# Kernel tuning notes

Hardware: AMD Instinct MI355X
Metric: run time of the kernel (lower is better)

## Reference

```python
import jax, jax.numpy as jnp
import numpy as np

B, S, H, W = 64, 32, 40, 64
SENS, UNITS, MOTOR, NA = 1283, 48, 4, 2
UNFOLDS = 6  # ncps LTC default ode_unfolds
EPS = 1e-8


def setup_inputs() -> dict:
    key = jax.random.key(0)
    ks = iter(jax.random.split(key, 40))
    u = lambda sh, lo, hi: jax.random.uniform(next(ks), sh, jnp.float32, lo, hi)
    inp = {}
    inp["depth_image"] = jax.random.uniform(next(ks), (B, S, H, W), jnp.float32)
    inp["relative_position"] = jax.random.normal(next(ks), (B, S, 3), jnp.float32)
    # CNN params (conv k3 s2 p1 + ReLU) x3: 1->32->64->32
    def cw(o, i):
        return jax.random.normal(next(ks), (o, i, 3, 3), jnp.float32) / np.sqrt(i * 9.0)
    inp["w1"], inp["b1"] = cw(32, 1), jnp.zeros((32,), jnp.float32)
    inp["w2"], inp["b2"] = cw(64, 32), jnp.zeros((64,), jnp.float32)
    inp["w3"], inp["b3"] = cw(32, 64), jnp.zeros((32,), jnp.float32)
    # LTC cell params (ncps init ranges)
    inp["input_w"] = jnp.ones((SENS,), jnp.float32)
    inp["input_b"] = jnp.zeros((SENS,), jnp.float32)
    inp["sens_w"] = u((SENS, UNITS), 0.001, 1.0)
    inp["sens_mu"] = u((SENS, UNITS), 0.3, 0.8)
    inp["sens_sigma"] = u((SENS, UNITS), 3.0, 8.0)
    inp["sens_erev"] = jnp.sign(jax.random.normal(next(ks), (SENS, UNITS)))
    inp["rec_w"] = u((UNITS, UNITS), 0.001, 1.0)
    inp["rec_mu"] = u((UNITS, UNITS), 0.3, 0.8)
    inp["rec_sigma"] = u((UNITS, UNITS), 3.0, 8.0)
    inp["rec_erev"] = jnp.sign(jax.random.normal(next(ks), (UNITS, UNITS)))
    inp["gleak"] = u((UNITS,), 0.001, 1.0)
    inp["vleak"] = u((UNITS,), -0.2, 0.2)
    inp["cm"] = u((UNITS,), 0.4, 0.6)
    inp["out_w"] = jnp.ones((MOTOR,), jnp.float32)
    inp["out_b"] = jnp.zeros((MOTOR,), jnp.float32)
    inp["head_w"] = jax.random.normal(next(ks), (MOTOR, NA), jnp.float32) * 0.5
    inp["head_b"] = jnp.zeros((NA,), jnp.float32)
    inp["sens_mask"] = (jax.random.uniform(next(ks), (SENS, UNITS)) < 0.3).astype(jnp.int32)
    inp["rec_mask"] = (jax.random.uniform(next(ks), (UNITS, UNITS)) < 0.3).astype(jnp.int32)
    return inp


def _conv(x, w, b):
    y = jax.lax.conv_general_dilated(x, w, (2, 2), [(1, 1), (1, 1)],
                                     dimension_numbers=("NCHW", "OIHW", "NCHW"))
    return jax.nn.relu(y + b[None, :, None, None])


def reference(depth_image, relative_position, w1, b1, w2, b2, w3, b3,
              input_w, input_b, sens_w, sens_mu, sens_sigma, sens_erev,
              rec_w, rec_mu, rec_sigma, rec_erev, gleak, vleak, cm,
              out_w, out_b, head_w, head_b, sens_mask, rec_mask):
    b, s = depth_image.shape[:2]
    x = depth_image.reshape(b * s, 1, H, W)
    x = _conv(_conv(_conv(x, w1, b1), w2, b2), w3, b3)  # [b*s,32,5,8]
    feat = x.reshape(b, s, -1)  # [b,s,1280]
    seq = jnp.concatenate([feat, relative_position.reshape(b, s, -1)], axis=2)  # [b,s,1283]

    sp = jax.nn.softplus
    smask = sens_mask.astype(seq.dtype)
    rmask = rec_mask.astype(seq.dtype)
    cm_t = sp(cm) * UNFOLDS          # cm / (elapsed_time / ode_unfolds), dt=1
    gl = sp(gleak)
    sw_pos = sp(sens_w) * smask
    rw_pos = sp(rec_w) * rmask

    def step(v, xt):  # xt: [b, SENS]
        I = xt * input_w + input_b
        # sensory synapse activations: [b, SENS, UNITS]
        sa = sw_pos * jax.nn.sigmoid(sens_sigma * (I[:, :, None] - sens_mu))
        w_num_s = (sa * sens_erev).sum(1)  # [b, UNITS]
        w_den_s = sa.sum(1)
        def unfold(v, _):
            ra = rw_pos * jax.nn.sigmoid(rec_sigma * (v[:, :, None] - rec_mu))
            num = cm_t * v + gl * vleak + (ra * rec_erev).sum(1) + w_num_s
            den = cm_t + gl + ra.sum(1) + w_den_s
            return num / (den + EPS), None
        v, _ = jax.lax.scan(unfold, v, None, length=UNFOLDS)
        y = v[:, :MOTOR] * out_w + out_b  # motor neuron readout
        return v, y

    v0 = jnp.zeros((b, UNITS), seq.dtype)
    _, ys = jax.lax.scan(step, v0, jnp.swapaxes(seq, 0, 1))  # [s, b, MOTOR]
    pooled = ys.mean(0)  # mean over seq dim
    return jnp.tanh(pooled @ head_w + head_b)  # [b, NA] action mean
```

## Files before the change

kernel.cpp:

```cpp
#include <hip/hip_runtime.h>
#include <hip/hip_bf16.h>


typedef __attribute__((ext_vector_type(8))) short bshort8;
typedef __attribute__((ext_vector_type(4))) float f32x4;

constexpr long OFF_SEQ  = 0;
constexpr long OFF_SP4  = 2627584;
constexpr long OFF_RP4  = 2873920;
constexpr long OFF_CM   = 2886208;
constexpr long OFF_W2B  = 2886400;
constexpr long OFF_W3B  = 2898688;
constexpr long OFF_PART = 2907904;

__device__ __forceinline__ float sp_(float x) {
    return fmaxf(x, 0.f) + log1pf(expf(-fabsf(x)));
}

__global__ void prep_kernel(const float* __restrict__ sens_w, const float* __restrict__ sens_mu,
                            const float* __restrict__ sens_sigma, const float* __restrict__ sens_erev,
                            const int* __restrict__ sens_mask,
                            const float* __restrict__ rec_w, const float* __restrict__ rec_mu,
                            const float* __restrict__ rec_sigma, const float* __restrict__ rec_erev,
                            const int* __restrict__ rec_mask,
                            const float* __restrict__ gleak, const float* __restrict__ vleak,
                            const float* __restrict__ cm,
                            const float* __restrict__ w2, const float* __restrict__ w3,
                            float* __restrict__ ws) {
    const float L2E = 1.4426950408889634f;
    int i = blockIdx.x * 256 + threadIdx.x;
    if (i < 61584) {
        float m  = sens_mask[i] ? 1.f : 0.f;
        float sw = sp_(sens_w[i]) * m;
        float sg = sens_sigma[i], mu = sens_mu[i];
        ((float4*)(ws + OFF_SP4))[i] =
            make_float4(-sg * L2E, sg * mu * L2E, sw * sens_erev[i], sw);
    } else if (i < 64656) {
        int q = i - 61584;
        int j = q >> 6, u = q & 63;
        float4 v = make_float4(0.f, 0.f, 0.f, 0.f);
        if (u < 48) {
            int idx = j * 48 + u;
            float m  = rec_mask[idx] ? 1.f : 0.f;
            float sw = sp_(rec_w[idx]) * m;
            float sg = rec_sigma[idx], mu = rec_mu[idx];
            v = make_float4(-sg * L2E, sg * mu * L2E, sw * rec_erev[idx], sw);
        }
        ((float4*)(ws + OFF_RP4))[q] = v;
    } else if (i < 64704) {
        int u = i - 64656;
        float g = sp_(gleak[u]);
        ws[OFF_CM + u]       = sp_(cm[u]) * 6.f;
        ws[OFF_CM + 64 + u]  = g;
        ws[OFF_CM + 128 + u] = g * vleak[u];
    } else if (i < 89280) {
        int n = i - 64704;
        int j = n & 7, l = (n >> 3) & 63, t2 = n >> 9;
        int wv = t2 & 3;
        int r  = t2 >> 2;
        int xp = r & 1, hk = r >> 1;
        int ky = hk % 3, h = hk / 3;
        int oc = wv * 16 + (l & 15);
        int kgB = l >> 4;
        int icl = (kgB & 1) * 8 + j;
        int ic = h * 16 + icl;
        int kx = 2 * xp + (kgB >> 1);
        float val = (kx == 3) ? 0.f : w2[((oc * 32 + ic) * 3 + ky) * 3 + kx];
        ((__hip_bfloat16*)(ws + OFF_W2B))[n] = __float2bfloat16(val);
    } else if (i < 107712) {
        int n = i - 89280;
        int j = n & 7, l = (n >> 3) & 63, t3 = n >> 9;
        int h = t3 & 1, u2 = t3 >> 1;
        int nt = u2 / 9, p = u2 % 9;
        int ky = p / 3, kx = p % 3;
        int oc = nt * 16 + (l & 15);
        int ic = h * 32 + (l >> 4) * 8 + j;
        ((__hip_bfloat16*)(ws + OFF_W3B))[n] =
            __float2bfloat16(w3[((oc * 64 + ic) * 3 + ky) * 3 + kx]);
    }
}

#define IMGB 0
#define C1H  5424
#define A2E  0
#define A2O  12672
#define SMB  28272

__global__ __launch_bounds__(256, 4) void cnn_kernel(
    const float* __restrict__ depth, const float* __restrict__ relpos,
    const float* __restrict__ w1, const float* __restrict__ b1,
    const float* __restrict__ b2, const float* __restrict__ b3,
    const __hip_bfloat16* __restrict__ w2b, const __hip_bfloat16* __restrict__ w3b,
    float* __restrict__ seq) {
    __shared__ __align__(16) char smraw[SMB];
    const int t = threadIdx.x;
    const int img = blockIdx.x;
    const int l = t & 63;
    const int wvu = __builtin_amdgcn_readfirstlane(t >> 6);
    const int m = l & 15, kg = l >> 4;

    for (int i = t; i < 7068; i += 256) ((uint*)smraw)[i] = 0u;
    __syncthreads();
    for (int i = t; i < 1280; i += 256) {
        int pos = 2 * i;
        int h = pos >> 6, w = pos & 63;
        float2 d = *(const float2*)(depth + (long)img * 2560 + pos);
        __hip_bfloat162 pk = __float22bfloat162_rn(d);
        *(__hip_bfloat162*)(smraw + IMGB + ((h + 1) * 66 + (w + 2)) * 2) = pk;
    }
    __syncthreads();

    const __hip_bfloat16* imgp = (const __hip_bfloat16*)(smraw + IMGB);
    f32x4 acc[10];
    {
        float bias = b2[wvu * 16 + m];
#pragma unroll
        for (int mt = 0; mt < 10; ++mt) acc[mt] = (f32x4){bias, bias, bias, bias};
    }

#pragma unroll 1
    for (int h = 0; h < 2; ++h) {
        const int ocb = h * 16 + wvu * 4;
        float wv4[4][9], bv4[4];
#pragma unroll
        for (int j = 0; j < 4; ++j) {
            bv4[j] = b1[ocb + j];
#pragma unroll
            for (int k = 0; k < 9; ++k) wv4[j][k] = w1[(ocb + j) * 9 + k];
        }
#pragma unroll 1
        for (int i = 0; i < 10; ++i) {
            int p = l + (i << 6);
            int y1 = p >> 5, x1 = p & 31;
            float xin[9];
#pragma unroll
            for (int ky = 0; ky < 3; ++ky)
#pragma unroll
                for (int kx = 0; kx < 3; ++kx)
                    xin[ky * 3 + kx] = __bfloat162float(imgp[(2 * y1 + ky) * 66 + 2 * x1 + kx + 1]);
            float o[4];
#pragma unroll
            for (int j = 0; j < 4; ++j) {
                float a = bv4[j];
#pragma unroll
                for (int k = 0; k < 9; ++k) a = fmaf(wv4[j][k], xin[k], a);
                o[j] = fmaxf(a, 0.f);
            }
            char* cb = smraw + C1H + (((y1 + 1) * 34) + (x1 + 1)) * 32 + wvu * 8;
            *(__hip_bfloat162*)cb       = __float22bfloat162_rn(make_float2(o[0], o[1]));
            *(__hip_bfloat162*)(cb + 4) = __float22bfloat162_rn(make_float2(o[2], o[3]));
        }
        bshort8 Bh[6];
#pragma unroll
        for (int f = 0; f < 6; ++f)
            Bh[f] = *(const bshort8*)(w2b + (((h * 6 + f) * 4 + wvu) * 64 + l) * 8);
        __syncthreads();
#pragma unroll
        for (int ky = 0; ky < 3; ++ky) {
#pragma unroll
            for (int xp = 0; xp < 2; ++xp) {
                bshort8 Bp = Bh[ky * 2 + xp];
                const char* base = smraw + C1H + (ky * 34 + 2 * m + 2 * xp + (kg >> 1)) * 32 + (kg & 1) * 16;
#pragma unroll
                for (int mt = 0; mt < 10; ++mt) {
                    bshort8 A = *(const bshort8*)(base + mt * 2176);
                    acc[mt] = __builtin_amdgcn_mfma_f32_16x16x32_bf16(A, Bp, acc[mt], 0, 0, 0);
                }
            }
        }
        __syncthreads();
    }

    for (int i = t; i < 6336; i += 256) ((uint*)smraw)[i] = 0u;
    __syncthreads();
    {
        int oc = wvu * 16 + m;
        int q = oc >> 3, sub = oc & 7;
#pragma unroll
        for (int mt = 0; mt < 10; ++mt) {
            int row = mt + 1;
#pragma unroll
            for (int reg = 0; reg < 4; ++reg) {
                int x2 = kg * 4 + reg;
                int odd = x2 & 1;
                int xi = odd ? ((x2 + 1) >> 1) : (x2 >> 1);
                char* ab = smraw + (odd ? A2O : A2E);
                float v = fmaxf(acc[mt][reg], 0.f);
                *(__hip_bfloat16*)(ab + (((q * 11 + row) * 9 + xi) * 8 + sub) * 2) = __float2bfloat16(v);
            }
        }
    }
    __syncthreads();

    {
        const int nt = wvu & 1;
        const bool two = wvu < 2;
        f32x4 c3a = (f32x4){0.f, 0.f, 0.f, 0.f};
        f32x4 c3b = (f32x4){0.f, 0.f, 0.f, 0.f};
        const int xb = m & 7, yb = m >> 3;
#pragma unroll
        for (int p = 0; p < 9; ++p) {
            int ky = p / 3, kx = p % 3;
            const char* arr = smraw + ((kx == 1) ? A2E : A2O);
            int xi3 = xb + (kx == 2);
#pragma unroll
            for (int h = 0; h < 2; ++h) {
                bshort8 B = *(const bshort8*)(w3b + (((nt * 9 + p) * 2 + h) * 64 + l) * 8);
                int q = h * 4 + kg;
                const char* base = arr + ((q * 11 + 2 * yb + ky) * 9 + xi3) * 16;
                if (two) {
                    bshort8 A0 = *(const bshort8*)(base);
                    c3a = __builtin_amdgcn_mfma_f32_16x16x32_bf16(A0, B, c3a, 0, 0, 0);
                    bshort8 A2 = *(const bshort8*)(base + 1152);
                    c3b = __builtin_amdgcn_mfma_f32_16x16x32_bf16(A2, B, c3b, 0, 0, 0);
                } else {
                    bshort8 A1 = *(const bshort8*)(base + 576);
                    c3a = __builtin_amdgcn_mfma_f32_16x16x32_bf16(A1, B, c3a, 0, 0, 0);
                }
            }
        }
        __syncthreads();
        float* sb = (float*)smraw;
        int oc = nt * 16 + m;
        float bv = b3[oc];
        int ob40 = oc * 40;
        if (two) {
#pragma unroll
            for (int reg = 0; reg < 4; ++reg) {
                sb[ob40 + kg * 4 + reg] = fmaxf(c3a[reg] + bv, 0.f);
                int px2 = 32 + kg * 4 + reg;
                if (px2 < 40) sb[ob40 + px2] = fmaxf(c3b[reg] + bv, 0.f);
            }
        } else {
#pragma unroll
            for (int reg = 0; reg < 4; ++reg)
                sb[ob40 + 16 + kg * 4 + reg] = fmaxf(c3a[reg] + bv, 0.f);
        }
        __syncthreads();
        for (int i = t; i < 1283; i += 256)
            seq[(long)img * 1283 + i] = (i < 1280) ? sb[i] : relpos[img * 3 + (i - 1280)];
    }
}

__global__ __launch_bounds__(768) void sensory_kernel(
    const float* __restrict__ sp, const float* __restrict__ seq,
    const float* __restrict__ iw, const float* __restrict__ ibias,
    float2* __restrict__ part) {
    const float4* P4 = (const float4*)sp;
    __shared__ __align__(16) char sbuf[49152];
    float*  IT  = (float*)sbuf;
    float2* red = (float2*)sbuf;
    const int t = threadIdx.x;
    const int pb = blockIdx.x * 8;

    for (int p = 0; p < 8; ++p)
        for (int k = t; k < 1283; k += 768)
            IT[k * 8 + p] = fmaf(seq[(long)(pb + p) * 1283 + k], iw[k], ibias[k]);
    __syncthreads();

    const int u = t % 48, kg = t / 48;
    float2 acc[8];
#pragma unroll
    for (int p = 0; p < 8; ++p) acc[p] = make_float2(0.f, 0.f);

#pragma unroll 2
    for (int i = 0; i < 81; ++i) {
        int k = kg + 16 * i;
        if (k < 1283) {
            float4 pv = P4[k * 48 + u];
            float4 Ia = *(const float4*)&IT[k * 8];
            float4 Ib = *(const float4*)&IT[k * 8 + 4];
            float r0 = __builtin_amdgcn_rcpf(1.f + __builtin_amdgcn_exp2f(fmaf(pv.x, Ia.x, pv.y)));
            float r1 = __builtin_amdgcn_rcpf(1.f + __builtin_amdgcn_exp2f(fmaf(pv.x, Ia.y, pv.y)));
            float r2 = __builtin_amdgcn_rcpf(1.f + __builtin_amdgcn_exp2f(fmaf(pv.x, Ia.z, pv.y)));
            float r3 = __builtin_amdgcn_rcpf(1.f + __builtin_amdgcn_exp2f(fmaf(pv.x, Ia.w, pv.y)));
            float r4 = __builtin_amdgcn_rcpf(1.f + __builtin_amdgcn_exp2f(fmaf(pv.x, Ib.x, pv.y)));
            float r5 = __builtin_amdgcn_rcpf(1.f + __builtin_amdgcn_exp2f(fmaf(pv.x, Ib.y, pv.y)));
            float r6 = __builtin_amdgcn_rcpf(1.f + __builtin_amdgcn_exp2f(fmaf(pv.x, Ib.z, pv.y)));
            float r7 = __builtin_amdgcn_rcpf(1.f + __builtin_amdgcn_exp2f(fmaf(pv.x, Ib.w, pv.y)));
            acc[0].x = fmaf(pv.z, r0, acc[0].x); acc[0].y = fmaf(pv.w, r0, acc[0].y);
            acc[1].x = fmaf(pv.z, r1, acc[1].x); acc[1].y = fmaf(pv.w, r1, acc[1].y);
            acc[2].x = fmaf(pv.z, r2, acc[2].x); acc[2].y = fmaf(pv.w, r2, acc[2].y);
            acc[3].x = fmaf(pv.z, r3, acc[3].x); acc[3].y = fmaf(pv.w, r3, acc[3].y);
            acc[4].x = fmaf(pv.z, r4, acc[4].x); acc[4].y = fmaf(pv.w, r4, acc[4].y);
            acc[5].x = fmaf(pv.z, r5, acc[5].x); acc[5].y = fmaf(pv.w, r5, acc[5].y);
            acc[6].x = fmaf(pv.z, r6, acc[6].x); acc[6].y = fmaf(pv.w, r6, acc[6].y);
            acc[7].x = fmaf(pv.z, r7, acc[7].x); acc[7].y = fmaf(pv.w, r7, acc[7].y);
        }
    }
    __syncthreads();
#pragma unroll
    for (int p = 0; p < 8; ++p) red[(kg * 8 + p) * 48 + u] = acc[p];
    __syncthreads();
    if (t < 384) {
        int p = t / 48, uu = t - p * 48;
        float sn = 0.f, sd = 0.f;
#pragma unroll
        for (int g = 0; g < 16; ++g) {
            float2 rr = red[(g * 8 + p) * 48 + uu];
            sn += rr.x; sd += rr.y;
        }
        part[(long)(pb + p) * 48 + uu] = make_float2(sn, sd);
    }
}

__global__ __launch_bounds__(256) void recurrent_kernel(
    const float* __restrict__ rp, const float* __restrict__ cmglv,
    const float2* __restrict__ part,
    const float* __restrict__ out_w, const float* __restrict__ out_b,
    const float* __restrict__ head_w, const float* __restrict__ head_b,
    float* __restrict__ outp) {
    const float4* RP4 = (const float4*)rp;
    __shared__ float2 WL[32 * 48];
    __shared__ float2 red[2][4][64];
    __shared__ float ym[4];
    const int t = threadIdx.x, b = blockIdx.x;
    const int u = t & 63;
    const int jg = __builtin_amdgcn_readfirstlane(t >> 6);
    const int j0 = jg * 12;
    const bool uval = u < 48;
    float4 rpj[12];
#pragma unroll
    for (int jj = 0; jj < 12; ++jj) rpj[jj] = RP4[(j0 + jj) * 64 + u];
    for (int i = t; i < 1536; i += 256) WL[i] = part[(long)b * 1536 + i];
    float cmt = 0.f, gl = 0.f, glv = 0.f;
    if (uval) { cmt = cmglv[u]; gl = cmglv[64 + u]; glv = cmglv[128 + u]; }
    float ow = 0.f, ob = 0.f;
    if (jg == 0 && u < 4) { ow = out_w[u]; ob = out_b[u]; }
    __syncthreads();

    float vn = 0.f;
    float yacc = 0.f;
    int buf = 0;
    for (int s = 0; s < 32; ++s) {
        float2 wnd = uval ? WL[s * 48 + u] : make_float2(0.f, 0.f);
#pragma unroll 1
        for (int unf = 0; unf < 6; ++unf) {
            float pn = 0.f, pd = 0.f;
#pragma unroll
            for (int jj = 0; jj < 12; ++jj) {
                float vj = __shfl(vn, j0 + jj, 64);
                float r = __builtin_amdgcn_rcpf(1.f + __builtin_amdgcn_exp2f(fmaf(rpj[jj].x, vj, rpj[jj].y)));
                pn = fmaf(rpj[jj].z, r, pn);
                pd = fmaf(rpj[jj].w, r, pd);
            }
            red[buf][jg][u] = make_float2(pn, pd);
            __syncthreads();
            float2 r0 = red[buf][0][u], r1 = red[buf][1][u];
            float2 r2 = red[buf][2][u], r3 = red[buf][3][u];
            float sn = r0.x + r1.x + r2.x + r3.x;
            float sd = r0.y + r1.y + r2.y + r3.y;
            float num = fmaf(cmt, vn, glv) + sn + wnd.x;
            float den = cmt + gl + sd + wnd.y;
            vn = uval ? num * __builtin_amdgcn_rcpf(den + 1e-8f) : 0.f;
            buf ^= 1;
        }
        if (jg == 0 && u < 4) yacc = fmaf(vn, ow, yacc) + ob;
    }
    if (jg == 0 && u < 4) ym[u] = yacc;
    __syncthreads();
    if (t < 2) {
        const float inv = 1.f / 32.f;
        float o = ym[0] * inv * head_w[t] + ym[1] * inv * head_w[2 + t] +
                  ym[2] * inv * head_w[4 + t] + ym[3] * inv * head_w[6 + t] + head_b[t];
        outp[b * 2 + t] = tanhf(o);
    }
}

extern "C" void kernel_launch(void* const* d_in, const int* in_sizes, int n_in,
                              void* d_out, int out_size, void* d_ws, size_t ws_size,
                              hipStream_t stream) {
    const float* depth      = (const float*)d_in[0];
    const float* relpos     = (const float*)d_in[1];
    const float* w1         = (const float*)d_in[2];
    const float* b1         = (const float*)d_in[3];
    const float* w2         = (const float*)d_in[4];
    const float* b2         = (const float*)d_in[5];
    const float* w3         = (const float*)d_in[6];
    const float* b3         = (const float*)d_in[7];
    const float* iw         = (const float*)d_in[8];
    const float* ibias      = (const float*)d_in[9];
    const float* sens_w     = (const float*)d_in[10];
    const float* sens_mu    = (const float*)d_in[11];
    const float* sens_sigma = (const float*)d_in[12];
    const float* sens_erev  = (const float*)d_in[13];
    const float* rec_w      = (const float*)d_in[14];
    const float* rec_mu     = (const float*)d_in[15];
    const float* rec_sigma  = (const float*)d_in[16];
    const float* rec_erev   = (const float*)d_in[17];
    const float* gleak      = (const float*)d_in[18];
    const float* vleak      = (const float*)d_in[19];
    const float* cm         = (const float*)d_in[20];
    const float* out_w      = (const float*)d_in[21];
    const float* out_b      = (const float*)d_in[22];
    const float* head_w     = (const float*)d_in[23];
    const float* head_b     = (const float*)d_in[24];
    const int*   sens_mask  = (const int*)d_in[25];
    const int*   rec_mask   = (const int*)d_in[26];

    float* ws  = (float*)d_ws;
    float* out = (float*)d_out;

    prep_kernel<<<477, 256, 0, stream>>>(sens_w, sens_mu, sens_sigma, sens_erev, sens_mask,
                                         rec_w, rec_mu, rec_sigma, rec_erev, rec_mask,
                                         gleak, vleak, cm, w2, w3, ws);
    cnn_kernel<<<2048, 256, 0, stream>>>(depth, relpos, w1, b1, b2, b3,
                                         (const __hip_bfloat16*)(ws + OFF_W2B),
                                         (const __hip_bfloat16*)(ws + OFF_W3B),
                                         ws + OFF_SEQ);
    sensory_kernel<<<256, 768, 0, stream>>>(ws + OFF_SP4, ws + OFF_SEQ, iw, ibias,
                                            (float2*)(ws + OFF_PART));
    recurrent_kernel<<<64, 256, 0, stream>>>(ws + OFF_RP4, ws + OFF_CM,
                                             (const float2*)(ws + OFF_PART),
                                             out_w, out_b, head_w, head_b, out);
}
```

Baseline: 307.5 us.

## Run recurrent LTC kernel as a single wavefront per batch, removing barriers

The recurrent kernel now uses one 64-lane wavefront per batch element, and each lane loops over all 48 presynaptic units instead of splitting them across four wavefronts. This removes the per-unfold shared-memory reduction and __syncthreads on the serial 192-step critical path. In exchange, each lane does four times the sigmoid work per unfold and holds 48 float4 parameters (192 VGPRs) in registers, which raises register pressure and the chance of spilling.

Result: slower. 428.1 us (+39.3%).

```diff
diff --git a/kernel.cpp b/kernel.cpp
--- a/kernel.cpp
+++ b/kernel.cpp
@@ -304,7 +304,7 @@
     }
 }
 
-__global__ __launch_bounds__(256) void recurrent_kernel(
+__global__ __launch_bounds__(64) void recurrent_kernel(
     const float* __restrict__ rp, const float* __restrict__ cmglv,
     const float2* __restrict__ part,
     const float* __restrict__ out_w, const float* __restrict__ out_b,
@@ -312,52 +312,41 @@
     float* __restrict__ outp) {
     const float4* RP4 = (const float4*)rp;
     __shared__ float2 WL[32 * 48];
-    __shared__ float2 red[2][4][64];
     __shared__ float ym[4];
     const int t = threadIdx.x, b = blockIdx.x;
-    const int u = t & 63;
-    const int jg = __builtin_amdgcn_readfirstlane(t >> 6);
-    const int j0 = jg * 12;
+    const int u = t;
     const bool uval = u < 48;
-    float4 rpj[12];
-#pragma unroll
-    for (int jj = 0; jj < 12; ++jj) rpj[jj] = RP4[(j0 + jj) * 64 + u];
-    for (int i = t; i < 1536; i += 256) WL[i] = part[(long)b * 1536 + i];
+    float4 rpj[48];
+#pragma unroll
+    for (int j = 0; j < 48; ++j) rpj[j] = RP4[j * 64 + u];
+    for (int i = t; i < 1536; i += 64) WL[i] = part[(long)b * 1536 + i];
     float cmt = 0.f, gl = 0.f, glv = 0.f;
     if (uval) { cmt = cmglv[u]; gl = cmglv[64 + u]; glv = cmglv[128 + u]; }
     float ow = 0.f, ob = 0.f;
-    if (jg == 0 && u < 4) { ow = out_w[u]; ob = out_b[u]; }
+    if (u < 4) { ow = out_w[u]; ob = out_b[u]; }
     __syncthreads();
 
     float vn = 0.f;
     float yacc = 0.f;
-    int buf = 0;
     for (int s = 0; s < 32; ++s) {
         float2 wnd = uval ? WL[s * 48 + u] : make_float2(0.f, 0.f);
 #pragma unroll 1
         for (int unf = 0; unf < 6; ++unf) {
             float pn = 0.f, pd = 0.f;
 #pragma unroll
-            for (int jj = 0; jj < 12; ++jj) {
-                float vj = __shfl(vn, j0 + jj, 64);
-                float r = __builtin_amdgcn_rcpf(1.f + __builtin_amdgcn_exp2f(fmaf(rpj[jj].x, vj, rpj[jj].y)));
-                pn = fmaf(rpj[jj].z, r, pn);
-                pd = fmaf(rpj[jj].w, r, pd);
-            }
-            red[buf][jg][u] = make_float2(pn, pd);
-            __syncthreads();
-            float2 r0 = red[buf][0][u], r1 = red[buf][1][u];
-            float2 r2 = red[buf][2][u], r3 = red[buf][3][u];
-            float sn = r0.x + r1.x + r2.x + r3.x;
-            float sd = r0.y + r1.y + r2.y + r3.y;
-            float num = fmaf(cmt, vn, glv) + sn + wnd.x;
-            float den = cmt + gl + sd + wnd.y;
+            for (int j = 0; j < 48; ++j) {
+                float vj = __shfl(vn, j, 64);
+                float r = __builtin_amdgcn_rcpf(1.f + __builtin_amdgcn_exp2f(fmaf(rpj[j].x, vj, rpj[j].y)));
+                pn = fmaf(rpj[j].z, r, pn);
+                pd = fmaf(rpj[j].w, r, pd);
+            }
+            float num = fmaf(cmt, vn, glv) + pn + wnd.x;
+            float den = cmt + gl + pd + wnd.y;
             vn = uval ? num * __builtin_amdgcn_rcpf(den + 1e-8f) : 0.f;
-            buf ^= 1;
-        }
-        if (jg == 0 && u < 4) yacc = fmaf(vn, ow, yacc) + ob;
-    }
-    if (jg == 0 && u < 4) ym[u] = yacc;
+        }
+        if (u < 4) yacc = fmaf(vn, ow, yacc) + ob;
+    }
+    if (u < 4) ym[u] = yacc;
     __syncthreads();
     if (t < 2) {
         const float inv = 1.f / 32.f;
@@ -410,7 +399,7 @@
                                          ws + OFF_SEQ);
     sensory_kernel<<<256, 768, 0, stream>>>(ws + OFF_SP4, ws + OFF_SEQ, iw, ibias,
                                             (float2*)(ws + OFF_PART));
-    recurrent_kernel<<<64, 256, 0, stream>>>(ws + OFF_RP4, ws + OFF_CM,
-                                             (const float2*)(ws + OFF_PART),
-                                             out_w, out_b, head_w, head_b, out);
-}
+    recurrent_kernel<<<64, 64, 0, stream>>>(ws + OFF_RP4, ws + OFF_CM,
+                                            (const float2*)(ws + OFF_PART),
+                                            out_w, out_b, head_w, head_b, out);
+}
```
